# Kernel tuning notes

Hardware: AMD Instinct MI355X
Metric: run time of the kernel (lower is better)

The kernel has to match this reference:

```python
import jax, jax.numpy as jnp
import numpy as np

N_NODES = 100000
N_EDGES = 600000
D = 128
HEADS = 8
REL = 9
N_GRAPHS = 64


def _relconv(h, coeff, basis, w_loop, b, src, dst, etypes, n_nodes):
    # DGL RelGraphConv, basis regularizer (num_bases == num_rels), sum aggregation,
    # self-loop, bias, relu activation (dropout inactive at eval).
    W = jnp.einsum('rb,bio->rio', coeff, basis)  # [REL, D, D]
    hsrc = h[src]                                # [E, D] gather
    msg = jnp.zeros((hsrc.shape[0], W.shape[2]), h.dtype)
    for r in range(REL):  # small fixed relation set
        msg = msg + jnp.where((etypes == r)[:, None], hsrc @ W[r], 0.0)
    agg = jax.ops.segment_sum(msg, dst, num_segments=n_nodes)
    return jax.nn.relu(agg + h @ w_loop + b)


def _graph_norm(x, seg, n_graphs, w, b, ms):
    # scatter-based per-subgraph normalization (graphNorm)
    counts = jax.ops.segment_sum(jnp.ones((x.shape[0],), x.dtype), seg, num_segments=n_graphs)[:, None]
    mean = jax.ops.segment_sum(x, seg, num_segments=n_graphs) / counts
    sub = x - mean[seg] * ms
    var = jax.ops.segment_sum(sub * sub, seg, num_segments=n_graphs) / counts
    std = jnp.sqrt(var + 1e-6)
    return w * sub / std[seg] + b


def _layer_norm(x, g, b):
    mu = x.mean(-1, keepdims=True)
    v = jnp.mean((x - mu) ** 2, -1, keepdims=True)
    return g * (x - mu) / jnp.sqrt(v + 1e-5) + b


def _forward(h, src, dst, etypes, seg, num_graphs,
             q_coeff, q_basis, q_loop, q_bias,
             k_coeff, k_basis, k_loop, k_bias,
             v_coeff, v_basis, v_loop, v_bias,
             o_w, o_b, gn1_w, gn1_b, gn1_ms, ln1_g, ln1_b,
             gn2_w, gn2_b, gn2_ms, ffn1_w, ffn1_b, ffn2_w, ffn2_b,
             ln2_g, ln2_b):
    n = h.shape[0]
    hn = _graph_norm(h, seg, num_graphs, gn1_w, gn1_b, gn1_ms)
    Q = _relconv(hn, q_coeff, q_basis, q_loop, q_bias, src, dst, etypes, n)
    K = _relconv(hn, k_coeff, k_basis, k_loop, k_bias, src, dst, etypes, n)
    V = _relconv(hn, v_coeff, v_basis, v_loop, v_bias, src, dst, etypes, n)
    dh = D // HEADS
    Qh = Q.reshape(n, HEADS, dh)
    Kh = K.reshape(n, HEADS, dh)
    Vh = V.reshape(n, HEADS, dh)
    # edge dot-product attention: score_e = <K[src], Q[dst]> per head
    score = (Kh[src] * Qh[dst]).sum(-1, keepdims=True)            # [E, H, 1]
    score = jnp.exp(jnp.clip(score / np.float32(np.sqrt(dh)), -10.0, 10.0))
    wV = jax.ops.segment_sum(Vh[src] * score, dst, num_segments=n)  # [N, H, dh]
    z = jax.ops.segment_sum(score, dst, num_segments=n)             # [N, H, 1]
    attn = (wV / (z + 1e-6)).reshape(n, D)
    hO = attn @ o_w + o_b
    h1 = _layer_norm(hO, ln1_g, ln1_b)
    h2 = _graph_norm(h1, seg, num_graphs, gn2_w, gn2_b, gn2_ms)
    h3 = jax.nn.relu(h2 @ ffn1_w + ffn1_b) @ ffn2_w + ffn2_b
    return _layer_norm(h3, ln2_g, ln2_b)


def setup_inputs() -> dict:
    key = jax.random.key(0)
    ks = jax.random.split(key, 32)
    s = np.float32(1.0 / np.sqrt(D))
    inp = {
        'h': jax.random.normal(ks[0], (N_NODES, D), jnp.float32),
        'src': jax.random.randint(ks[1], (N_EDGES,), 0, N_NODES),
        'dst': jax.random.randint(ks[2], (N_EDGES,), 0, N_NODES),
        'etypes': jax.random.randint(ks[3], (N_EDGES,), 0, REL),
        'seg': jnp.sort(jax.random.randint(ks[4], (N_NODES,), 0, N_GRAPHS)),
        'num_graphs': N_GRAPHS,
    }
    def lin(k, i, o):
        return jax.random.normal(k, (i, o), jnp.float32) / np.float32(np.sqrt(i))
    for idx, nm in enumerate(['q', 'k', 'v']):
        base = 5 + idx * 4
        inp[nm + '_coeff'] = jax.random.normal(ks[base], (REL, REL), jnp.float32) / np.float32(np.sqrt(REL))
        inp[nm + '_basis'] = jax.random.normal(ks[base + 1], (REL, D, D), jnp.float32) * s
        inp[nm + '_loop'] = lin(ks[base + 2], D, D)
        inp[nm + '_bias'] = jnp.zeros((D,), jnp.float32)
    inp['o_w'] = lin(ks[17], D, D)
    inp['o_b'] = jnp.zeros((D,), jnp.float32)
    for nm in ['gn1', 'gn2']:
        inp[nm + '_w'] = jnp.ones((D,), jnp.float32)
        inp[nm + '_b'] = jnp.zeros((D,), jnp.float32)
        inp[nm + '_ms'] = jnp.ones((D,), jnp.float32)
    inp['ln1_g'] = jnp.ones((D,), jnp.float32)
    inp['ln1_b'] = jnp.zeros((D,), jnp.float32)
    inp['ln2_g'] = jnp.ones((D,), jnp.float32)
    inp['ln2_b'] = jnp.zeros((D,), jnp.float32)
    inp['ffn1_w'] = lin(ks[18], D, 2 * D)
    inp['ffn1_b'] = jnp.zeros((2 * D,), jnp.float32)
    inp['ffn2_w'] = lin(ks[19], 2 * D, D)
    inp['ffn2_b'] = jnp.zeros((D,), jnp.float32)
    return inp


def reference(h, src, dst, etypes, seg, num_graphs,
              q_coeff, q_basis, q_loop, q_bias,
              k_coeff, k_basis, k_loop, k_bias,
              v_coeff, v_basis, v_loop, v_bias,
              o_w, o_b, gn1_w, gn1_b, gn1_ms, ln1_g, ln1_b,
              gn2_w, gn2_b, gn2_ms, ffn1_w, ffn1_b, ffn2_w, ffn2_b,
              ln2_g, ln2_b):
    return _forward(h, src, dst, etypes, seg, num_graphs,
                    q_coeff, q_basis, q_loop, q_bias,
                    k_coeff, k_basis, k_loop, k_bias,
                    v_coeff, v_basis, v_loop, v_bias,
                    o_w, o_b, gn1_w, gn1_b, gn1_ms, ln1_g, ln1_b,
                    gn2_w, gn2_b, gn2_ms, ffn1_w, ffn1_b, ffn2_w, ffn2_b,
                    ln2_g, ln2_b)
```

## Files before the change

kernel.cpp:

```cpp
#include <hip/hip_runtime.h>
#include <math.h>

#define N_NODES 100000
#define N_EDGES 600000
#define D 128
#define REL 9
#define NG 64
#define NK9 (N_NODES * REL)
#define C1LD 264

typedef float f32x4 __attribute__((ext_vector_type(4)));
typedef _Float16 f16x8 __attribute__((ext_vector_type(8)));
typedef _Float16 h16x2 __attribute__((ext_vector_type(2)));

__device__ __forceinline__ ushort f2h(float x) {
    union { _Float16 h; ushort u; } c; c.h = (_Float16)x; return c.u;
}
__device__ __forceinline__ float h2f(ushort u) {
    union { ushort u; _Float16 h; } c; c.u = u; return (float)c.h;
}

__device__ __forceinline__ void ld16(const ushort* g, ushort* l) {
    __builtin_amdgcn_global_load_lds(
        (const __attribute__((address_space(1))) unsigned int*)g,
        (__attribute__((address_space(3))) unsigned int*)l, 16, 0, 0);
}

__device__ __forceinline__ int lbound(const int* __restrict__ a, int n, int key) {
    int lo = 0, hi = n;
    while (lo < hi) { int mid = (lo + hi) >> 1; if (a[mid] < key) lo = mid + 1; else hi = mid; }
    return lo;
}

__global__ void hist9_kernel(const int* __restrict__ dst, const int* __restrict__ ety,
                             int* __restrict__ cnt9) {
    int e = blockIdx.x * 256 + threadIdx.x;
    if (e < N_EDGES) atomicAdd(&cnt9[dst[e] * REL + ety[e]], 1);
}

__global__ void scan1_8(const int* __restrict__ cnt, int* __restrict__ excl,
                        int* __restrict__ bsum, int n) {
    __shared__ int s[1024];
    int tid = threadIdx.x;
    int base = blockIdx.x * 8192 + tid * 8;
    int v[8]; int sum = 0;
#pragma unroll
    for (int j = 0; j < 8; ++j) { v[j] = (base + j < n) ? cnt[base + j] : 0; sum += v[j]; }
    s[tid] = sum;
    __syncthreads();
    for (int off = 1; off < 1024; off <<= 1) {
        int t = (tid >= off) ? s[tid - off] : 0;
        __syncthreads();
        s[tid] += t;
        __syncthreads();
    }
    int run = s[tid] - sum;
#pragma unroll
    for (int j = 0; j < 8; ++j) { if (base + j < n) excl[base + j] = run; run += v[j]; }
    if (tid == 1023) bsum[blockIdx.x] = s[1023];
}

__global__ void scan2_kernel(int* __restrict__ bsum, int nb) {
    __shared__ int s[128];
    int tid = threadIdx.x;
    int v = (tid < nb) ? bsum[tid] : 0;
    s[tid] = v;
    __syncthreads();
    for (int off = 1; off < 128; off <<= 1) {
        int t = (tid >= off) ? s[tid - off] : 0;
        __syncthreads();
        s[tid] += t;
        __syncthreads();
    }
    if (tid < nb) bsum[tid] = s[tid] - v;
}

__global__ void scan3_8(int* __restrict__ excl, const int* __restrict__ bsum, int n, int total) {
    int base = blockIdx.x * 8192 + threadIdx.x * 8;
    int add = bsum[blockIdx.x];
#pragma unroll
    for (int j = 0; j < 8; ++j) if (base + j < n) excl[base + j] += add;
    if (blockIdx.x == 0 && threadIdx.x == 0) excl[n] = total;
}

__global__ void scatter9_kernel(const int* __restrict__ src, const int* __restrict__ dst,
                                const int* __restrict__ ety, const int* __restrict__ rstart,
                                int* __restrict__ cur9, int* __restrict__ ssrc,
                                int* __restrict__ setp) {
    int e = blockIdx.x * 256 + threadIdx.x;
    if (e < N_EDGES) {
        int t = ety[e];
        int key = dst[e] * REL + t;
        int pos = rstart[key] + atomicAdd(&cur9[key], 1);
        ssrc[pos] = src[e];
        setp[pos] = t;
    }
}

__global__ __launch_bounds__(256)
void gn_stats(const float* __restrict__ x, const int* __restrict__ seg,
              float* __restrict__ gsum, float* __restrict__ gsumsq) {
    __shared__ float redS[8][128];
    __shared__ float redQ[8][128];
    int t = threadIdx.x;
    int c4 = (t & 31) * 4;
    int rr = t >> 5;
    int n0 = blockIdx.x * 128;
    int nend = min(n0 + 128, N_NODES);
    int len = nend - n0;
    int gfirst = seg[n0];
    int glast = seg[nend - 1];
    for (int g = gfirst; g <= glast; ++g) {
        int lo = (g == gfirst) ? n0 : n0 + lbound(seg + n0, len, g);
        int hi = (g == glast) ? nend : n0 + lbound(seg + n0, len, g + 1);
        float s0 = 0.f, s1 = 0.f, s2 = 0.f, s3 = 0.f;
        float q0 = 0.f, q1 = 0.f, q2 = 0.f, q3 = 0.f;
        for (int n = lo + rr; n < hi; n += 8) {
            float4 v = *(const float4*)&x[(size_t)n * D + c4];
            s0 += v.x; q0 += v.x * v.x;
            s1 += v.y; q1 += v.y * v.y;
            s2 += v.z; q2 += v.z * v.z;
            s3 += v.w; q3 += v.w * v.w;
        }
        redS[rr][c4 + 0] = s0; redS[rr][c4 + 1] = s1;
        redS[rr][c4 + 2] = s2; redS[rr][c4 + 3] = s3;
        redQ[rr][c4 + 0] = q0; redQ[rr][c4 + 1] = q1;
        redQ[rr][c4 + 2] = q2; redQ[rr][c4 + 3] = q3;
        __syncthreads();
        if (t < 128) {
            float ts = 0.f, tq = 0.f;
#pragma unroll
            for (int ph = 0; ph < 8; ++ph) { ts += redS[ph][t]; tq += redQ[ph][t]; }
            atomicAdd(&gsum[g * D + t], ts);
            atomicAdd(&gsumsq[g * D + t], tq);
        }
        __syncthreads();
    }
}

__global__ __launch_bounds__(256)
void gn_stats_h(const ushort* __restrict__ x, const int* __restrict__ seg,
                float* __restrict__ gsum, float* __restrict__ gsumsq) {
    __shared__ float redS[8][128];
    __shared__ float redQ[8][128];
    int t = threadIdx.x;
    int c4 = (t & 31) * 4;
    int rr = t >> 5;
    int n0 = blockIdx.x * 128;
    int nend = min(n0 + 128, N_NODES);
    int len = nend - n0;
    int gfirst = seg[n0];
    int glast = seg[nend - 1];
    for (int g = gfirst; g <= glast; ++g) {
        int lo = (g == gfirst) ? n0 : n0 + lbound(seg + n0, len, g);
        int hi = (g == glast) ? nend : n0 + lbound(seg + n0, len, g + 1);
        float s0 = 0.f, s1 = 0.f, s2 = 0.f, s3 = 0.f;
        float q0 = 0.f, q1 = 0.f, q2 = 0.f, q3 = 0.f;
        for (int n = lo + rr; n < hi; n += 8) {
            ushort4 u = *(const ushort4*)&x[(size_t)n * D + c4];
            float v0 = h2f(u.x), v1 = h2f(u.y), v2 = h2f(u.z), v3 = h2f(u.w);
            s0 += v0; q0 += v0 * v0;
            s1 += v1; q1 += v1 * v1;
            s2 += v2; q2 += v2 * v2;
            s3 += v3; q3 += v3 * v3;
        }
        redS[rr][c4 + 0] = s0; redS[rr][c4 + 1] = s1;
        redS[rr][c4 + 2] = s2; redS[rr][c4 + 3] = s3;
        redQ[rr][c4 + 0] = q0; redQ[rr][c4 + 1] = q1;
        redQ[rr][c4 + 2] = q2; redQ[rr][c4 + 3] = q3;
        __syncthreads();
        if (t < 128) {
            float ts = 0.f, tq = 0.f;
#pragma unroll
            for (int ph = 0; ph < 8; ++ph) { ts += redS[ph][t]; tq += redQ[ph][t]; }
            atomicAdd(&gsum[g * D + t], ts);
            atomicAdd(&gsumsq[g * D + t], tq);
        }
        __syncthreads();
    }
}

__global__ void gn_final(const float* __restrict__ gsum, const float* __restrict__ gsumsq,
                         const int* __restrict__ seg, const float* __restrict__ w,
                         const float* __restrict__ b, const float* __restrict__ ms,
                         float* __restrict__ sc, float* __restrict__ off) {
    int g = blockIdx.x, ch = threadIdx.x;
    int lo = lbound(seg, N_NODES, g), hi = lbound(seg, N_NODES, g + 1);
    float cnt = (float)max(hi - lo, 1);
    float mean = gsum[g * D + ch] / cnt;
    float mm = mean * ms[ch];
    float var = gsumsq[g * D + ch] / cnt - 2.f * mm * mean + mm * mm;
    float rstd = rsqrtf(var + 1e-6f);
    float s = w[ch] * rstd;
    sc[g * D + ch] = s;
    off[g * D + ch] = b[ch] - s * mm;
}

__global__ __launch_bounds__(256)
void gn_apply(const float* __restrict__ x, const int* __restrict__ seg,
              const float* __restrict__ sc, const float* __restrict__ off,
              ushort* __restrict__ outhf) {
    int t = blockIdx.x * 256 + threadIdx.x;
    int n = t >> 6;
    if (n >= N_NODES) return;
    int ch = (t & 63) * 2;
    int g = seg[n];
    float2 xv = *(const float2*)&x[(size_t)n * D + ch];
    float2 s2 = *(const float2*)&sc[g * D + ch];
    float2 o2 = *(const float2*)&off[g * D + ch];
    ushort2 o;
    o.x = f2h(s2.x * xv.x + o2.x);
    o.y = f2h(s2.y * xv.y + o2.y);
    *(ushort2*)&outhf[(size_t)n * D + ch] = o;
}

__global__ __launch_bounds__(256)
void gn_apply_h(const ushort* __restrict__ x, const int* __restrict__ seg,
                const float* __restrict__ sc, const float* __restrict__ off,
                ushort* __restrict__ outhf) {
    int t = blockIdx.x * 256 + threadIdx.x;
    int n = t >> 6;
    if (n >= N_NODES) return;
    int ch = (t & 63) * 2;
    int g = seg[n];
    ushort2 xv = *(const ushort2*)&x[(size_t)n * D + ch];
    float2 s2 = *(const float2*)&sc[g * D + ch];
    float2 o2 = *(const float2*)&off[g * D + ch];
    ushort2 o;
    o.x = f2h(s2.x * h2f(xv.x) + o2.x);
    o.y = f2h(s2.y * h2f(xv.y) + o2.y);
    *(ushort2*)&outhf[(size_t)n * D + ch] = o;
}

__global__ void build_bt_qkv3(const float* __restrict__ c0, const float* __restrict__ c1,
                              const float* __restrict__ c2, const float* __restrict__ b0,
                              const float* __restrict__ b1, const float* __restrict__ b2,
                              const float* __restrict__ l0, const float* __restrict__ l1,
                              const float* __restrict__ l2, const float* __restrict__ i0,
                              const float* __restrict__ i1, const float* __restrict__ i2,
                              ushort* __restrict__ Btqkv, float* __restrict__ biasq) {
    int pj = blockIdx.y;
    const float* coeff  = pj == 0 ? c0 : (pj == 1 ? c1 : c2);
    const float* basis  = pj == 0 ? b0 : (pj == 1 ? b1 : b2);
    const float* loop_w = pj == 0 ? l0 : (pj == 1 ? l1 : l2);
    const float* bin    = pj == 0 ? i0 : (pj == 1 ? i1 : i2);
    ushort* Bt = Btqkv + (size_t)pj * 128 * 1280;
    int t = blockIdx.x * 256 + threadIdx.x;
    if (t < 128) biasq[pj * 128 + t] = bin[t];
    if (t >= 128 * 1280) return;
    int o = t / 1280;
    int k = t - o * 1280;
    float v;
    if (k < 128) {
        v = loop_w[k * 128 + o];
    } else {
        int kk = k - 128;
        int r = kk >> 7, i = kk & 127;
        v = 0.f;
#pragma unroll
        for (int b = 0; b < REL; ++b)
            v += coeff[r * REL + b] * basis[((size_t)b * 128 + i) * 128 + o];
    }
    Bt[(size_t)o * 1280 + k] = f2h(v);
}

__global__ void transpose_cast3(const float* __restrict__ o_w, ushort* __restrict__ Bto,
                                const float* __restrict__ f1, ushort* __restrict__ Btf1,
                                const float* __restrict__ f2, ushort* __restrict__ Btf2) {
    int t = blockIdx.x * 256 + threadIdx.x;
    if (t < 16384) {
        int n = t >> 7, k = t & 127;
        Bto[(size_t)n * 128 + k] = f2h(o_w[(size_t)k * 128 + n]);
    } else if (t < 49152) {
        int u = t - 16384;
        int n = u >> 7, k = u & 127;
        Btf1[(size_t)n * 128 + k] = f2h(f1[(size_t)k * 256 + n]);
    } else if (t < 81920) {
        int u = t - 49152;
        int n = u >> 8, k = u & 255;
        Btf2[(size_t)n * 256 + k] = f2h(f2[(size_t)k * 128 + n]);
    }
}

__global__ __launch_bounds__(256)
void s_pass(const ushort* __restrict__ hnhf, const int* __restrict__ ssrc,
            const int* __restrict__ setp, const int* __restrict__ rstart,
            ushort* __restrict__ Ab, int c0, int c1) {
    int n = c0 + ((blockIdx.x * 256 + threadIdx.x) >> 6);
    if (n >= c1) return;
    int lane = threadIdx.x & 63;
    int e0 = rstart[n * REL], e1 = rstart[n * REL + REL];
    h16x2 a0 = (h16x2)0, a1 = (h16x2)0, a2 = (h16x2)0, a3 = (h16x2)0, a4 = (h16x2)0;
    h16x2 a5 = (h16x2)0, a6 = (h16x2)0, a7 = (h16x2)0, a8 = (h16x2)0;
#define ACC(rr, hv) switch (rr) { \
        case 0: a0 += hv; break; case 1: a1 += hv; break; case 2: a2 += hv; break; \
        case 3: a3 += hv; break; case 4: a4 += hv; break; case 5: a5 += hv; break; \
        case 6: a6 += hv; break; case 7: a7 += hv; break; default: a8 += hv; break; }
    int e = e0;
    for (; e + 4 <= e1; e += 4) {
        int s0 = ssrc[e], s1 = ssrc[e + 1], s2 = ssrc[e + 2], s3 = ssrc[e + 3];
        int r0 = __builtin_amdgcn_readfirstlane(setp[e]);
        int r1 = __builtin_amdgcn_readfirstlane(setp[e + 1]);
        int r2 = __builtin_amdgcn_readfirstlane(setp[e + 2]);
        int r3 = __builtin_amdgcn_readfirstlane(setp[e + 3]);
        h16x2 hv0 = *(const h16x2*)&hnhf[(size_t)s0 * D + 2 * lane];
        h16x2 hv1 = *(const h16x2*)&hnhf[(size_t)s1 * D + 2 * lane];
        h16x2 hv2 = *(const h16x2*)&hnhf[(size_t)s2 * D + 2 * lane];
        h16x2 hv3 = *(const h16x2*)&hnhf[(size_t)s3 * D + 2 * lane];
        ACC(r0, hv0)
        ACC(r1, hv1)
        ACC(r2, hv2)
        ACC(r3, hv3)
    }
    for (; e < e1; ++e) {
        int s0 = ssrc[e];
        int r0 = __builtin_amdgcn_readfirstlane(setp[e]);
        h16x2 hv0 = *(const h16x2*)&hnhf[(size_t)s0 * D + 2 * lane];
        ACC(r0, hv0)
    }
#undef ACC
    ushort* arow = Ab + (size_t)(n - c0) * 1152;
#define ST(r) *(h16x2*)&arow[r * 128 + 2 * lane] = a##r;
    ST(0) ST(1) ST(2) ST(3) ST(4) ST(5) ST(6) ST(7) ST(8)
#undef ST
}

__global__ __launch_bounds__(512)
void mfma_gemm384(const ushort* __restrict__ A1, const ushort* __restrict__ Ab, int M,
                  const ushort* __restrict__ Bt, const float* __restrict__ bias,
                  ushort* __restrict__ Cout) {
    __shared__ ushort As[128 * 64];
    __shared__ ushort Bs[384 * 64];
    const int tid = threadIdx.x;
    const int lane = tid & 63;
    const int wave = tid >> 6;
    const int wm = wave & 1, wn = wave >> 1;
    const int quad = lane >> 4, l16 = lane & 15;
    const int row0 = blockIdx.x * 128;

    const ushort* sA1[2];
    const ushort* sA2[2];
#pragma unroll
    for (int i = 0; i < 2; ++i) {
        int rs = (wave * 2 + i) * 8 + (lane >> 3);
        int kg = (lane & 7) ^ (rs & 7);
        int ra = row0 + rs; if (ra >= M) ra = M - 1;
        sA1[i] = A1 + (size_t)ra * 128 + kg * 8;
        sA2[i] = Ab + (size_t)ra * 1152 + kg * 8;
    }
    const ushort* sB[6];
#pragma unroll
    for (int i = 0; i < 6; ++i) {
        int rs = (wave * 6 + i) * 8 + (lane >> 3);
        int kg = (lane & 7) ^ (rs & 7);
        sB[i] = Bt + (size_t)rs * 1280 + kg * 8;
    }

    f32x4 acc[4][6];
#pragma unroll
    for (int i = 0; i < 4; ++i)
#pragma unroll
        for (int j = 0; j < 6; ++j) acc[i][j] = (f32x4){0.f, 0.f, 0.f, 0.f};

    for (int kc = 0; kc < 1280; kc += 64) {
#pragma unroll
        for (int i = 0; i < 6; ++i) ld16(sB[i] + kc, &Bs[(wave * 6 + i) * 512]);
#pragma unroll
        for (int i = 0; i < 2; ++i) {
            const ushort* as = (kc < 128) ? (sA1[i] + kc) : (sA2[i] + (kc - 128));
            ld16(as, &As[(wave * 2 + i) * 512]);
        }
        __syncthreads();
#pragma unroll
        for (int h = 0; h < 2; ++h) {
            f16x8 af[4], bf[6];
#pragma unroll
            for (int i = 0; i < 4; ++i) {
                int r = wm * 64 + i * 16 + l16;
                af[i] = *(const f16x8*)&As[r * 64 + (((h * 4 + quad) ^ (r & 7)) * 8)];
            }
#pragma unroll
            for (int j = 0; j < 6; ++j) {
                int c = wn * 96 + j * 16 + l16;
                bf[j] = *(const f16x8*)&Bs[c * 64 + (((h * 4 + quad) ^ (c & 7)) * 8)];
            }
#pragma unroll
            for (int i = 0; i < 4; ++i)
#pragma unroll
                for (int j = 0; j < 6; ++j)
                    acc[i][j] = __builtin_amdgcn_mfma_f32_16x16x32_f16(af[i], bf[j], acc[i][j], 0, 0, 0);
        }
        __syncthreads();
    }

#pragma unroll
    for (int i = 0; i < 4; ++i) {
        int gr0 = wm * 64 + i * 16 + quad * 4 + row0;
#pragma unroll
        for (int r = 0; r < 4; ++r) {
            int gr = gr0 + r;
            if (gr >= M) continue;
#pragma unroll
            for (int j = 0; j < 6; ++j) {
                int gcol = wn * 96 + j * 16 + l16;
                float v = acc[i][j][r] + bias[gcol];
                v = fmaxf(v, 0.f);
                Cout[(size_t)gr * 384 + gcol] = f2h(v);
            }
        }
    }
}

template<bool F16OUT>
__global__ __launch_bounds__(256, 3)
void mfma_gemm_ln(const ushort* __restrict__ A, int lda, int M,
                  const ushort* __restrict__ Bt, int K,
                  const float* __restrict__ bias, const float* __restrict__ lng,
                  const float* __restrict__ lnb, void* __restrict__ Cout) {
    __shared__ ushort As[128 * 64];
    __shared__ ushort Bs[128 * 64];
    __shared__ float rsum[2][128];
    __shared__ float rsq[2][128];
    const int tid = threadIdx.x;
    const int lane = tid & 63;
    const int wave = tid >> 6;
    const int wm = wave & 1, wn = wave >> 1;
    const int quad = lane >> 4, l16 = lane & 15;
    const int row0 = blockIdx.y * 128;

    const ushort* sA[4];
    const ushort* sB[4];
#pragma unroll
    for (int i = 0; i < 4; ++i) {
        int rs = (wave * 4 + i) * 8 + (lane >> 3);
        int kg = (lane & 7) ^ (rs & 7);
        int ra = row0 + rs; if (ra >= M) ra = M - 1;
        sA[i] = A + (size_t)ra * lda + kg * 8;
        sB[i] = Bt + (size_t)rs * K + kg * 8;
    }

    f32x4 acc[4][4];
#pragma unroll
    for (int i = 0; i < 4; ++i)
#pragma unroll
        for (int j = 0; j < 4; ++j) acc[i][j] = (f32x4){0.f, 0.f, 0.f, 0.f};

    for (int kc = 0; kc < K; kc += 64) {
#pragma unroll
        for (int i = 0; i < 4; ++i) {
            ld16(sA[i] + kc, &As[(wave * 4 + i) * 512]);
            ld16(sB[i] + kc, &Bs[(wave * 4 + i) * 512]);
        }
        __syncthreads();
#pragma unroll
        for (int h = 0; h < 2; ++h) {
            f16x8 af[4], bf[4];
#pragma unroll
            for (int i = 0; i < 4; ++i) {
                int r = wm * 64 + i * 16 + l16;
                af[i] = *(const f16x8*)&As[r * 64 + (((h * 4 + quad) ^ (r & 7)) * 8)];
                int c = wn * 64 + i * 16 + l16;
                bf[i] = *(const f16x8*)&Bs[c * 64 + (((h * 4 + quad) ^ (c & 7)) * 8)];
            }
#pragma unroll
            for (int i = 0; i < 4; ++i)
#pragma unroll
                for (int j = 0; j < 4; ++j)
                    acc[i][j] = __builtin_amdgcn_mfma_f32_16x16x32_f16(af[i], bf[j], acc[i][j], 0, 0, 0);
        }
        __syncthreads();
    }

#pragma unroll
    for (int i = 0; i < 4; ++i) {
#pragma unroll
        for (int r = 0; r < 4; ++r) {
            float s = 0.f, q = 0.f;
#pragma unroll
            for (int j = 0; j < 4; ++j) {
                float v = acc[i][j][r] + bias[wn * 64 + j * 16 + l16];
                s += v; q += v * v;
            }
            s += __shfl_xor(s, 1); q += __shfl_xor(q, 1);
            s += __shfl_xor(s, 2); q += __shfl_xor(q, 2);
            s += __shfl_xor(s, 4); q += __shfl_xor(q, 4);
            s += __shfl_xor(s, 8); q += __shfl_xor(q, 8);
            if (l16 == 0) {
                int row = wm * 64 + i * 16 + quad * 4 + r;
                rsum[wn][row] = s;
                rsq[wn][row] = q;
            }
        }
    }
    __syncthreads();

#pragma unroll
    for (int i = 0; i < 4; ++i) {
#pragma unroll
        for (int r = 0; r < 4; ++r) {
            int row = wm * 64 + i * 16 + quad * 4 + r;
            int grow = row0 + row;
            if (grow >= M) continue;
            float tot = rsum[0][row] + rsum[1][row];
            float tq  = rsq[0][row] + rsq[1][row];
            float mu = tot * (1.f / 128.f);
            float var = tq * (1.f / 128.f) - mu * mu;
            float rstd = rsqrtf(var + 1e-5f);
#pragma unroll
            for (int j = 0; j < 4; ++j) {
                int gcol = wn * 64 + j * 16 + l16;
                float v = acc[i][j][r] + bias[gcol];
                float o = lng[gcol] * (v - mu) * rstd + lnb[gcol];
                if (F16OUT) ((ushort*)Cout)[(size_t)grow * 128 + gcol] = f2h(o);
                else        ((float*)Cout)[(size_t)grow * 128 + gcol] = o;
            }
        }
    }
}

__global__ __launch_bounds__(512)
void ffn_fused(const ushort* __restrict__ A, int M,
               const ushort* __restrict__ B1t, const float* __restrict__ b1,
               const ushort* __restrict__ B2t, const float* __restrict__ b2,
               const float* __restrict__ lng, const float* __restrict__ lnb,
               float* __restrict__ Cout) {
    extern __shared__ ushort sh[];
    ushort* As   = sh;
    ushort* Bs   = sh + 64 * 64;
    ushort* C1s  = sh + 64 * 64 + 256 * 64;
    float*  rsum = (float*)(C1s + 64 * C1LD);
    float*  rsq  = rsum + 4 * 64;
    const int tid = threadIdx.x;
    const int lane = tid & 63;
    const int wave = tid >> 6;
    const int wm = wave & 1, wn = wave >> 1;
    const int quad = lane >> 4, l16 = lane & 15;
    const int row0 = blockIdx.x * 64;

    {
        int rsA = wave * 8 + (lane >> 3);
        int kgA = (lane & 7) ^ (rsA & 7);
        int raA = row0 + rsA; if (raA >= M) raA = M - 1;
        const ushort* sA = A + (size_t)raA * 128 + kgA * 8;
        const ushort* sB[4];
#pragma unroll
        for (int i = 0; i < 4; ++i) {
            int rs = (wave * 4 + i) * 8 + (lane >> 3);
            int kg = (lane & 7) ^ (rs & 7);
            sB[i] = B1t + (size_t)rs * 128 + kg * 8;
        }
        f32x4 acc[2][4];
#pragma unroll
        for (int i = 0; i < 2; ++i)
#pragma unroll
            for (int j = 0; j < 4; ++j) acc[i][j] = (f32x4){0.f, 0.f, 0.f, 0.f};

        for (int kc = 0; kc < 128; kc += 64) {
#pragma unroll
            for (int i = 0; i < 4; ++i) ld16(sB[i] + kc, &Bs[(wave * 4 + i) * 512]);
            ld16(sA + kc, &As[wave * 512]);
            __syncthreads();
#pragma unroll
            for (int h = 0; h < 2; ++h) {
                f16x8 af[2], bf[4];
#pragma unroll
                for (int i = 0; i < 2; ++i) {
                    int r = wm * 32 + i * 16 + l16;
                    af[i] = *(const f16x8*)&As[r * 64 + (((h * 4 + quad) ^ (r & 7)) * 8)];
                }
#pragma unroll
                for (int j = 0; j < 4; ++j) {
                    int c = wn * 64 + j * 16 + l16;
                    bf[j] = *(const f16x8*)&Bs[c * 64 + (((h * 4 + quad) ^ (c & 7)) * 8)];
                }
#pragma unroll
                for (int i = 0; i < 2; ++i)
#pragma unroll
                    for (int j = 0; j < 4; ++j)
                        acc[i][j] = __builtin_amdgcn_mfma_f32_16x16x32_f16(af[i], bf[j], acc[i][j], 0, 0, 0);
            }
            __syncthreads();
        }

#pragma unroll
        for (int i = 0; i < 2; ++i) {
            int lr0 = wm * 32 + i * 16 + quad * 4;
#pragma unroll
            for (int r = 0; r < 4; ++r) {
                int row = lr0 + r;
#pragma unroll
                for (int j = 0; j < 4; ++j) {
                    int col = wn * 64 + j * 16 + l16;
                    float v = acc[i][j][r] + b1[col];
                    v = fmaxf(v, 0.f);
                    C1s[row * C1LD + col] = f2h(v);
                }
            }
        }
    }
    __syncthreads();

    {
        const ushort* sB[2];
#pragma unroll
        for (int i = 0; i < 2; ++i) {
            int rs = (wave * 2 + i) * 8 + (lane >> 3);
            int kg = (lane & 7) ^ (rs & 7);
            sB[i] = B2t + (size_t)rs * 256 + kg * 8;
        }
        f32x4 acc[2][2];
#pragma unroll
        for (int i = 0; i < 2; ++i)
#pragma unroll
            for (int j = 0; j < 2; ++j) acc[i][j] = (f32x4){0.f, 0.f, 0.f, 0.f};

        for (int kc = 0; kc < 256; kc += 64) {
#pragma unroll
            for (int i = 0; i < 2; ++i) ld16(sB[i] + kc, &Bs[(wave * 2 + i) * 512]);
            __syncthreads();
#pragma unroll
            for (int h = 0; h < 2; ++h) {
                f16x8 af[2], bf[2];
#pragma unroll
                for (int i = 0; i < 2; ++i) {
                    int r = wm * 32 + i * 16 + l16;
                    af[i] = *(const f16x8*)&C1s[r * C1LD + kc + ((h * 4 + quad) * 8)];
                }
#pragma unroll
                for (int j = 0; j < 2; ++j) {
                    int c = wn * 32 + j * 16 + l16;
                    bf[j] = *(const f16x8*)&Bs[c * 64 + (((h * 4 + quad) ^ (c & 7)) * 8)];
                }
#pragma unroll
                for (int i = 0; i < 2; ++i)
#pragma unroll
                    for (int j = 0; j < 2; ++j)
                        acc[i][j] = __builtin_amdgcn_mfma_f32_16x16x32_f16(af[i], bf[j], acc[i][j], 0, 0, 0);
            }
            __syncthreads();
        }

#pragma unroll
        for (int i = 0; i < 2; ++i) {
#pragma unroll
            for (int r = 0; r < 4; ++r) {
                float s = 0.f, q = 0.f;
#pragma unroll
                for (int j = 0; j < 2; ++j) {
                    float v = acc[i][j][r] + b2[wn * 32 + j * 16 + l16];
                    s += v; q += v * v;
                }
                s += __shfl_xor(s, 1); q += __shfl_xor(q, 1);
                s += __shfl_xor(s, 2); q += __shfl_xor(q, 2);
                s += __shfl_xor(s, 4); q += __shfl_xor(q, 4);
                s += __shfl_xor(s, 8); q += __shfl_xor(q, 8);
                if (l16 == 0) {
                    int row = wm * 32 + i * 16 + quad * 4 + r;
                    rsum[wn * 64 + row] = s;
                    rsq[wn * 64 + row] = q;
                }
            }
        }
        __syncthreads();

#pragma unroll
        for (int i = 0; i < 2; ++i) {
#pragma unroll
            for (int r = 0; r < 4; ++r) {
                int row = wm * 32 + i * 16 + quad * 4 + r;
                int grow = row0 + row;
                if (grow >= M) continue;
                float tot = rsum[row] + rsum[64 + row] + rsum[128 + row] + rsum[192 + row];
                float tq  = rsq[row] + rsq[64 + row] + rsq[128 + row] + rsq[192 + row];
                float mu = tot * (1.f / 128.f);
                float var = tq * (1.f / 128.f) - mu * mu;
                float rstd = rsqrtf(var + 1e-5f);
#pragma unroll
                for (int j = 0; j < 2; ++j) {
                    int gcol = wn * 32 + j * 16 + l16;
                    float v = acc[i][j][r] + b2[gcol];
                    float o = lng[gcol] * (v - mu) * rstd + lnb[gcol];
                    Cout[(size_t)grow * 128 + gcol] = o;
                }
            }
        }
    }
}

__global__ __launch_bounds__(256)
void attn_kernel(const ushort* __restrict__ C, const int* __restrict__ ssrc,
                 const int* __restrict__ rstart, ushort* __restrict__ attnhf) {
    int n = (blockIdx.x * 256 + threadIdx.x) >> 6;
    if (n >= N_NODES) return;
    int lane = threadIdx.x & 63;
    h16x2 qh = *(const h16x2*)&C[(size_t)n * 384 + 2 * lane];
    int e0 = rstart[n * REL], e1 = rstart[n * REL + REL];
    float wvx = 0.f, wvy = 0.f, z = 0.f;
    int e = e0;
    for (; e + 8 <= e1; e += 8) {
        int s[8];
#pragma unroll
        for (int j = 0; j < 8; ++j) s[j] = ssrc[e + j];
        h16x2 kk[8], vv[8];
#pragma unroll
        for (int j = 0; j < 8; ++j) kk[j] = *(const h16x2*)&C[(size_t)s[j] * 384 + 128 + 2 * lane];
#pragma unroll
        for (int j = 0; j < 8; ++j) vv[j] = *(const h16x2*)&C[(size_t)s[j] * 384 + 256 + 2 * lane];
        float d[8];
#pragma unroll
        for (int j = 0; j < 8; ++j) d[j] = __builtin_amdgcn_fdot2(kk[j], qh, 0.f, false);
#pragma unroll
        for (int j = 0; j < 8; ++j) d[j] += __shfl_xor(d[j], 1);
#pragma unroll
        for (int j = 0; j < 8; ++j) d[j] += __shfl_xor(d[j], 2);
#pragma unroll
        for (int j = 0; j < 8; ++j) d[j] += __shfl_xor(d[j], 4);
#pragma unroll
        for (int j = 0; j < 8; ++j) {
            float sc = __expf(fminf(fmaxf(d[j] * 0.25f, -10.f), 10.f));
            wvx += sc * (float)vv[j].x;
            wvy += sc * (float)vv[j].y;
            z += sc;
        }
    }
    for (; e + 4 <= e1; e += 4) {
        int s0 = ssrc[e], s1 = ssrc[e + 1], s2 = ssrc[e + 2], s3 = ssrc[e + 3];
        h16x2 k0 = *(const h16x2*)&C[(size_t)s0 * 384 + 128 + 2 * lane];
        h16x2 k1 = *(const h16x2*)&C[(size_t)s1 * 384 + 128 + 2 * lane];
        h16x2 k2 = *(const h16x2*)&C[(size_t)s2 * 384 + 128 + 2 * lane];
        h16x2 k3 = *(const h16x2*)&C[(size_t)s3 * 384 + 128 + 2 * lane];
        h16x2 v0 = *(const h16x2*)&C[(size_t)s0 * 384 + 256 + 2 * lane];
        h16x2 v1 = *(const h16x2*)&C[(size_t)s1 * 384 + 256 + 2 * lane];
        h16x2 v2 = *(const h16x2*)&C[(size_t)s2 * 384 + 256 + 2 * lane];
        h16x2 v3 = *(const h16x2*)&C[(size_t)s3 * 384 + 256 + 2 * lane];
        float d0 = __builtin_amdgcn_fdot2(k0, qh, 0.f, false);
        float d1 = __builtin_amdgcn_fdot2(k1, qh, 0.f, false);
        float d2 = __builtin_amdgcn_fdot2(k2, qh, 0.f, false);
        float d3 = __builtin_amdgcn_fdot2(k3, qh, 0.f, false);
        d0 += __shfl_xor(d0, 1); d1 += __shfl_xor(d1, 1);
        d2 += __shfl_xor(d2, 1); d3 += __shfl_xor(d3, 1);
        d0 += __shfl_xor(d0, 2); d1 += __shfl_xor(d1, 2);
        d2 += __shfl_xor(d2, 2); d3 += __shfl_xor(d3, 2);
        d0 += __shfl_xor(d0, 4); d1 += __shfl_xor(d1, 4);
        d2 += __shfl_xor(d2, 4); d3 += __shfl_xor(d3, 4);
        float sc0 = __expf(fminf(fmaxf(d0 * 0.25f, -10.f), 10.f));
        float sc1 = __expf(fminf(fmaxf(d1 * 0.25f, -10.f), 10.f));
        float sc2 = __expf(fminf(fmaxf(d2 * 0.25f, -10.f), 10.f));
        float sc3 = __expf(fminf(fmaxf(d3 * 0.25f, -10.f), 10.f));
        wvx += sc0 * (float)v0.x + sc1 * (float)v1.x;
        wvy += sc0 * (float)v0.y + sc1 * (float)v1.y;
        wvx += sc2 * (float)v2.x + sc3 * (float)v3.x;
        wvy += sc2 * (float)v2.y + sc3 * (float)v3.y;
        z += sc0 + sc1 + sc2 + sc3;
    }
    for (; e < e1; ++e) {
        int s0 = ssrc[e];
        h16x2 k0 = *(const h16x2*)&C[(size_t)s0 * 384 + 128 + 2 * lane];
        h16x2 v0 = *(const h16x2*)&C[(size_t)s0 * 384 + 256 + 2 * lane];
        float d0 = __builtin_amdgcn_fdot2(k0, qh, 0.f, false);
        d0 += __shfl_xor(d0, 1);
        d0 += __shfl_xor(d0, 2);
        d0 += __shfl_xor(d0, 4);
        float sc0 = __expf(fminf(fmaxf(d0 * 0.25f, -10.f), 10.f));
        wvx += sc0 * (float)v0.x;
        wvy += sc0 * (float)v0.y;
        z += sc0;
    }
    float inv = 1.f / (z + 1e-6f);
    ushort2 o;
    o.x = f2h(wvx * inv);
    o.y = f2h(wvy * inv);
    *(ushort2*)&attnhf[(size_t)n * D + 2 * lane] = o;
}

extern "C" void kernel_launch(void* const* d_in, const int* in_sizes, int n_in,
                              void* d_out, int out_size, void* d_ws, size_t ws_size,
                              hipStream_t stream) {
    (void)in_sizes; (void)n_in; (void)out_size;
    const float* h     = (const float*)d_in[0];
    const int*   src   = (const int*)d_in[1];
    const int*   dst   = (const int*)d_in[2];
    const int*   ety   = (const int*)d_in[3];
    const int*   seg   = (const int*)d_in[4];
    const float* coeffs[3] = {(const float*)d_in[6],  (const float*)d_in[10], (const float*)d_in[14]};
    const float* bases [3] = {(const float*)d_in[7],  (const float*)d_in[11], (const float*)d_in[15]};
    const float* loops [3] = {(const float*)d_in[8],  (const float*)d_in[12], (const float*)d_in[16]};
    const float* pbias [3] = {(const float*)d_in[9],  (const float*)d_in[13], (const float*)d_in[17]};
    const float* o_w   = (const float*)d_in[18];
    const float* o_b   = (const float*)d_in[19];
    const float* gn1_w = (const float*)d_in[20];
    const float* gn1_b = (const float*)d_in[21];
    const float* gn1_ms= (const float*)d_in[22];
    const float* gn2_w = (const float*)d_in[23];
    const float* gn2_b = (const float*)d_in[24];
    const float* gn2_ms= (const float*)d_in[25];
    const float* ln1_g = (const float*)d_in[26];
    const float* ln1_b = (const float*)d_in[27];
    const float* ln2_g = (const float*)d_in[28];
    const float* ln2_b = (const float*)d_in[29];
    const float* ffn1_w= (const float*)d_in[30];
    const float* ffn1_b= (const float*)d_in[31];
    const float* ffn2_w= (const float*)d_in[32];
    const float* ffn2_b= (const float*)d_in[33];

    char* p = (char*)d_ws;
    auto take = [&](size_t bytes) { char* r = p; p += (bytes + 255) & ~(size_t)255; return r; };
    int*    cnt9   = (int*)take((size_t)NK9 * 2 * 4);
    int*    cur9   = cnt9 + NK9;
    int*    rstart = (int*)take((size_t)(NK9 + 8) * 4);
    int*    bsum   = (int*)take(512);
    int*    ssrc   = (int*)take((size_t)N_EDGES * 4);
    int*    setp   = (int*)take((size_t)N_EDGES * 4);
    float*  gsum   = (float*)take((size_t)NG * D * 4 * 2);
    float*  gsumsq = gsum + NG * D;
    float*  gsc    = (float*)take((size_t)NG * D * 4);
    float*  goff   = (float*)take((size_t)NG * D * 4);
    ushort* Btqkv  = (ushort*)take((size_t)384 * 1280 * 2);
    float*  biasq  = (float*)take(384 * 4);
    ushort* Bto    = (ushort*)take((size_t)128 * 128 * 2);
    ushort* Btf1   = (ushort*)take((size_t)256 * 128 * 2);
    ushort* Btf2   = (ushort*)take((size_t)128 * 256 * 2);
    ushort* hnhf   = (ushort*)take((size_t)N_NODES * D * 2);
    ushort* attnhf = (ushort*)take((size_t)N_NODES * D * 2);
    ushort* h1hf   = (ushort*)take((size_t)N_NODES * D * 2);
    ushort* Cqkv   = (ushort*)take((size_t)N_NODES * 384 * 2);
    size_t used = (size_t)(p - (char*)d_ws);
    size_t avail = (ws_size > used) ? ws_size - used : 0;
    int NC = 1;
    if (avail < (size_t)N_NODES * 1152 * 2) NC = 4;
    if (NC == 4 && avail < ((size_t)(N_NODES / 4 + 1) * 1152 * 2)) NC = 8;
    ushort* Ab = (ushort*)p;
    const int chunk = (N_NODES + NC - 1) / NC;

    ushort* gn2hf  = Cqkv;

    const int EB = (N_EDGES + 255) / 256;
    const int KB = (NK9 + 8191) / 8192;
    const int WB = (N_NODES * 64 + 255) / 256;
    const int GB = (N_NODES + 127) / 128;
    const int RB = (N_NODES + 127) / 128;
    const int FB = (N_NODES + 63) / 64;

    hipMemsetAsync(cnt9, 0, (size_t)NK9 * 8, stream);
    hist9_kernel<<<EB, 256, 0, stream>>>(dst, ety, cnt9);
    scan1_8<<<KB, 1024, 0, stream>>>(cnt9, rstart, bsum, NK9);
    scan2_kernel<<<1, 128, 0, stream>>>(bsum, KB);
    scan3_8<<<KB, 1024, 0, stream>>>(rstart, bsum, NK9, N_EDGES);
    scatter9_kernel<<<EB, 256, 0, stream>>>(src, dst, ety, rstart, cur9, ssrc, setp);

    build_bt_qkv3<<<dim3(640, 3), 256, 0, stream>>>(
        coeffs[0], coeffs[1], coeffs[2], bases[0], bases[1], bases[2],
        loops[0], loops[1], loops[2], pbias[0], pbias[1], pbias[2], Btqkv, biasq);
    transpose_cast3<<<320, 256, 0, stream>>>(o_w, Bto, ffn1_w, Btf1, ffn2_w, Btf2);

    hipMemsetAsync(gsum, 0, (size_t)NG * D * 8, stream);
    gn_stats<<<GB, 256, 0, stream>>>(h, seg, gsum, gsumsq);
    gn_final<<<NG, 128, 0, stream>>>(gsum, gsumsq, seg, gn1_w, gn1_b, gn1_ms, gsc, goff);
    gn_apply<<<WB, 256, 0, stream>>>(h, seg, gsc, goff, hnhf);

    for (int c = 0; c < NC; ++c) {
        int c0 = c * chunk;
        int c1 = min(N_NODES, c0 + chunk);
        int rows = c1 - c0;
        if (rows <= 0) break;
        s_pass<<<(rows + 3) / 4, 256, 0, stream>>>(hnhf, ssrc, setp, rstart, Ab, c0, c1);
        mfma_gemm384<<<(rows + 127) / 128, 512, 0, stream>>>(
            hnhf + (size_t)c0 * 128, Ab, rows, Btqkv, biasq, Cqkv + (size_t)c0 * 384);
    }

    attn_kernel<<<WB, 256, 0, stream>>>(Cqkv, ssrc, rstart, attnhf);

    mfma_gemm_ln<true><<<dim3(1, RB), 256, 0, stream>>>(
        attnhf, 128, N_NODES, Bto, 128, o_b, ln1_g, ln1_b, h1hf);

    hipMemsetAsync(gsum, 0, (size_t)NG * D * 8, stream);
    gn_stats_h<<<GB, 256, 0, stream>>>(h1hf, seg, gsum, gsumsq);
    gn_final<<<NG, 128, 0, stream>>>(gsum, gsumsq, seg, gn2_w, gn2_b, gn2_ms, gsc, goff);
    gn_apply_h<<<WB, 256, 0, stream>>>(h1hf, seg, gsc, goff, gn2hf);

    const int FFN_LDS = (64 * 64 + 256 * 64 + 64 * C1LD) * 2 + 2 * 4 * 64 * 4;
    hipFuncSetAttribute((const void*)ffn_fused, hipFuncAttributeMaxDynamicSharedMemorySize, FFN_LDS);
    ffn_fused<<<FB, 512, FFN_LDS, stream>>>(
        gn2hf, N_NODES, Btf1, ffn1_b, Btf2, ffn2_b, ln2_g, ln2_b, (float*)d_out);
}
```

Before: 718.4 us.

## Derive relation type from CSR offsets and fuse graphNorm-2 apply into FFN load

Drops the per-edge relation-type array: scatter no longer writes it, and the aggregation pass works out each edge's relation by comparing the edge index against the node's nine sub-segment offsets. The second graphNorm apply kernel is removed, and the FFN kernel now normalises its A tile on the fly from h1 using the per-graph scale and offset. This saves one full node-feature write and read plus an edge array write and read. In exchange the FFN A loads become synchronous register loads with extra math instead of async direct-to-LDS copies, and the aggregation pass does more integer comparisons per edge.

```diff
diff --git a/kernel.cpp b/kernel.cpp
--- a/kernel.cpp
+++ b/kernel.cpp
@@ -85,15 +85,12 @@
 
 __global__ void scatter9_kernel(const int* __restrict__ src, const int* __restrict__ dst,
                                 const int* __restrict__ ety, const int* __restrict__ rstart,
-                                int* __restrict__ cur9, int* __restrict__ ssrc,
-                                int* __restrict__ setp) {
+                                int* __restrict__ cur9, int* __restrict__ ssrc) {
     int e = blockIdx.x * 256 + threadIdx.x;
     if (e < N_EDGES) {
-        int t = ety[e];
-        int key = dst[e] * REL + t;
+        int key = dst[e] * REL + ety[e];
         int pos = rstart[key] + atomicAdd(&cur9[key], 1);
         ssrc[pos] = src[e];
-        setp[pos] = t;
     }
 }
 
@@ -214,24 +211,6 @@
     *(ushort2*)&outhf[(size_t)n * D + ch] = o;
 }
 
-__global__ __launch_bounds__(256)
-void gn_apply_h(const ushort* __restrict__ x, const int* __restrict__ seg,
-                const float* __restrict__ sc, const float* __restrict__ off,
-                ushort* __restrict__ outhf) {
-    int t = blockIdx.x * 256 + threadIdx.x;
-    int n = t >> 6;
-    if (n >= N_NODES) return;
-    int ch = (t & 63) * 2;
-    int g = seg[n];
-    ushort2 xv = *(const ushort2*)&x[(size_t)n * D + ch];
-    float2 s2 = *(const float2*)&sc[g * D + ch];
-    float2 o2 = *(const float2*)&off[g * D + ch];
-    ushort2 o;
-    o.x = f2h(s2.x * h2f(xv.x) + o2.x);
-    o.y = f2h(s2.y * h2f(xv.y) + o2.y);
-    *(ushort2*)&outhf[(size_t)n * D + ch] = o;
-}
-
 __global__ void build_bt_qkv3(const float* __restrict__ c0, const float* __restrict__ c1,
                               const float* __restrict__ c2, const float* __restrict__ b0,
                               const float* __restrict__ b1, const float* __restrict__ b2,
@@ -284,14 +263,19 @@
 
 __global__ __launch_bounds__(256)
 void s_pass(const ushort* __restrict__ hnhf, const int* __restrict__ ssrc,
-            const int* __restrict__ setp, const int* __restrict__ rstart,
-            ushort* __restrict__ Ab, int c0, int c1) {
+            const int* __restrict__ rstart, ushort* __restrict__ Ab, int c0, int c1) {
     int n = c0 + ((blockIdx.x * 256 + threadIdx.x) >> 6);
     if (n >= c1) return;
     int lane = threadIdx.x & 63;
-    int e0 = rstart[n * REL], e1 = rstart[n * REL + REL];
+    const int* rp = rstart + n * REL;
+    int e0 = rp[0];
+    int rs1 = rp[1], rs2 = rp[2], rs3 = rp[3], rs4 = rp[4];
+    int rs5 = rp[5], rs6 = rp[6], rs7 = rp[7], rs8 = rp[8];
+    int e1 = rp[9];
     h16x2 a0 = (h16x2)0, a1 = (h16x2)0, a2 = (h16x2)0, a3 = (h16x2)0, a4 = (h16x2)0;
     h16x2 a5 = (h16x2)0, a6 = (h16x2)0, a7 = (h16x2)0, a8 = (h16x2)0;
+#define RELOF(ee) (((ee) >= rs1) + ((ee) >= rs2) + ((ee) >= rs3) + ((ee) >= rs4) + \
+                   ((ee) >= rs5) + ((ee) >= rs6) + ((ee) >= rs7) + ((ee) >= rs8))
 #define ACC(rr, hv) switch (rr) { \
         case 0: a0 += hv; break; case 1: a1 += hv; break; case 2: a2 += hv; break; \
         case 3: a3 += hv; break; case 4: a4 += hv; break; case 5: a5 += hv; break; \
@@ -299,10 +283,7 @@
     int e = e0;
     for (; e + 4 <= e1; e += 4) {
         int s0 = ssrc[e], s1 = ssrc[e + 1], s2 = ssrc[e + 2], s3 = ssrc[e + 3];
-        int r0 = __builtin_amdgcn_readfirstlane(setp[e]);
-        int r1 = __builtin_amdgcn_readfirstlane(setp[e + 1]);
-        int r2 = __builtin_amdgcn_readfirstlane(setp[e + 2]);
-        int r3 = __builtin_amdgcn_readfirstlane(setp[e + 3]);
+        int r0 = RELOF(e), r1 = RELOF(e + 1), r2 = RELOF(e + 2), r3 = RELOF(e + 3);
         h16x2 hv0 = *(const h16x2*)&hnhf[(size_t)s0 * D + 2 * lane];
         h16x2 hv1 = *(const h16x2*)&hnhf[(size_t)s1 * D + 2 * lane];
         h16x2 hv2 = *(const h16x2*)&hnhf[(size_t)s2 * D + 2 * lane];
@@ -314,11 +295,12 @@
     }
     for (; e < e1; ++e) {
         int s0 = ssrc[e];
-        int r0 = __builtin_amdgcn_readfirstlane(setp[e]);
+        int r0 = RELOF(e);
         h16x2 hv0 = *(const h16x2*)&hnhf[(size_t)s0 * D + 2 * lane];
         ACC(r0, hv0)
     }
 #undef ACC
+#undef RELOF
     ushort* arow = Ab + (size_t)(n - c0) * 1152;
 #define ST(r) *(h16x2*)&arow[r * 128 + 2 * lane] = a##r;
     ST(0) ST(1) ST(2) ST(3) ST(4) ST(5) ST(6) ST(7) ST(8)
@@ -519,7 +501,8 @@
 }
 
 __global__ __launch_bounds__(512)
-void ffn_fused(const ushort* __restrict__ A, int M,
+void ffn_fused(const ushort* __restrict__ h1, const int* __restrict__ seg,
+               const float* __restrict__ gsc, const float* __restrict__ goff, int M,
                const ushort* __restrict__ B1t, const float* __restrict__ b1,
                const ushort* __restrict__ B2t, const float* __restrict__ b2,
                const float* __restrict__ lng, const float* __restrict__ lnb,
@@ -541,7 +524,11 @@
         int rsA = wave * 8 + (lane >> 3);
         int kgA = (lane & 7) ^ (rsA & 7);
         int raA = row0 + rsA; if (raA >= M) raA = M - 1;
-        const ushort* sA = A + (size_t)raA * 128 + kgA * 8;
+        int gA = seg[raA];
+        const ushort* srcA = h1 + (size_t)raA * 128 + kgA * 8;
+        const float*  scp  = gsc + gA * 128 + kgA * 8;
+        const float*  offp = goff + gA * 128 + kgA * 8;
+        ushort* dstA = &As[wave * 512 + lane * 8];
         const ushort* sB[4];
 #pragma unroll
         for (int i = 0; i < 4; ++i) {
@@ -558,7 +545,24 @@
         for (int kc = 0; kc < 128; kc += 64) {
 #pragma unroll
             for (int i = 0; i < 4; ++i) ld16(sB[i] + kc, &Bs[(wave * 4 + i) * 512]);
-            ld16(sA + kc, &As[wave * 512]);
+            {
+                ushort4 u0 = *(const ushort4*)(srcA + kc);
+                ushort4 u1 = *(const ushort4*)(srcA + kc + 4);
+                float4 sc0 = *(const float4*)(scp + kc);
+                float4 sc1 = *(const float4*)(scp + kc + 4);
+                float4 of0 = *(const float4*)(offp + kc);
+                float4 of1 = *(const float4*)(offp + kc + 4);
+                f16x8 av;
+                av[0] = (_Float16)(sc0.x * h2f(u0.x) + of0.x);
+                av[1] = (_Float16)(sc0.y * h2f(u0.y) + of0.y);
+                av[2] = (_Float16)(sc0.z * h2f(u0.z) + of0.z);
+                av[3] = (_Float16)(sc0.w * h2f(u0.w) + of0.w);
+                av[4] = (_Float16)(sc1.x * h2f(u1.x) + of1.x);
+                av[5] = (_Float16)(sc1.y * h2f(u1.y) + of1.y);
+                av[6] = (_Float16)(sc1.z * h2f(u1.z) + of1.z);
+                av[7] = (_Float16)(sc1.w * h2f(u1.w) + of1.w);
+                *(f16x8*)dstA = av;
+            }
             __syncthreads();
 #pragma unroll
             for (int h = 0; h < 2; ++h) {
@@ -810,7 +814,6 @@
     int*    rstart = (int*)take((size_t)(NK9 + 8) * 4);
     int*    bsum   = (int*)take(512);
     int*    ssrc   = (int*)take((size_t)N_EDGES * 4);
-    int*    setp   = (int*)take((size_t)N_EDGES * 4);
     float*  gsum   = (float*)take((size_t)NG * D * 4 * 2);
     float*  gsumsq = gsum + NG * D;
     float*  gsc    = (float*)take((size_t)NG * D * 4);
@@ -832,8 +835,6 @@
     ushort* Ab = (ushort*)p;
     const int chunk = (N_NODES + NC - 1) / NC;
 
-    ushort* gn2hf  = Cqkv;
-
     const int EB = (N_EDGES + 255) / 256;
     const int KB = (NK9 + 8191) / 8192;
     const int WB = (N_NODES * 64 + 255) / 256;
@@ -846,7 +847,7 @@
     scan1_8<<<KB, 1024, 0, stream>>>(cnt9, rstart, bsum, NK9);
     scan2_kernel<<<1, 128, 0, stream>>>(bsum, KB);
     scan3_8<<<KB, 1024, 0, stream>>>(rstart, bsum, NK9, N_EDGES);
-    scatter9_kernel<<<EB, 256, 0, stream>>>(src, dst, ety, rstart, cur9, ssrc, setp);
+    scatter9_kernel<<<EB, 256, 0, stream>>>(src, dst, ety, rstart, cur9, ssrc);
 
     build_bt_qkv3<<<dim3(640, 3), 256, 0, stream>>>(
         coeffs[0], coeffs[1], coeffs[2], bases[0], bases[1], bases[2],
@@ -863,7 +864,7 @@
         int c1 = min(N_NODES, c0 + chunk);
         int rows = c1 - c0;
         if (rows <= 0) break;
-        s_pass<<<(rows + 3) / 4, 256, 0, stream>>>(hnhf, ssrc, setp, rstart, Ab, c0, c1);
+        s_pass<<<(rows + 3) / 4, 256, 0, stream>>>(hnhf, ssrc, rstart, Ab, c0, c1);
         mfma_gemm384<<<(rows + 127) / 128, 512, 0, stream>>>(
             hnhf + (size_t)c0 * 128, Ab, rows, Btqkv, biasq, Cqkv + (size_t)c0 * 384);
     }
@@ -876,10 +877,9 @@
     hipMemsetAsync(gsum, 0, (size_t)NG * D * 8, stream);
     gn_stats_h<<<GB, 256, 0, stream>>>(h1hf, seg, gsum, gsumsq);
     gn_final<<<NG, 128, 0, stream>>>(gsum, gsumsq, seg, gn2_w, gn2_b, gn2_ms, gsc, goff);
-    gn_apply_h<<<WB, 256, 0, stream>>>(h1hf, seg, gsc, goff, gn2hf);
 
     const int FFN_LDS = (64 * 64 + 256 * 64 + 64 * C1LD) * 2 + 2 * 4 * 64 * 4;
     hipFuncSetAttribute((const void*)ffn_fused, hipFuncAttributeMaxDynamicSharedMemorySize, FFN_LDS);
     ffn_fused<<<FB, 512, FFN_LDS, stream>>>(
-        gn2hf, N_NODES, Btf1, ffn1_b, Btf2, ffn2_b, ln2_g, ln2_b, (float*)d_out);
-}
+        h1hf, seg, gsc, goff, N_NODES, Btf1, ffn1_b, Btf2, ffn2_b, ln2_g, ln2_b, (float*)d_out);
+}
```

Measured after the change: 704.5 us. Within noise of the previous version (-1.9%).
